# Kernel tuning notes

Hardware: AMD Instinct MI355X
Metric: run time of the kernel (lower is better)

Reference implementation:

```python
import jax, jax.numpy as jnp
import numpy as np

TEMPERATURE = 0.05
EPS = 1e-6
N, D = 8192, 64


def setup_inputs() -> dict:
    key = jax.random.key(0)
    k1, k2 = jax.random.split(key)
    anchor_embeddings = jax.random.normal(k1, (N, D), dtype=jnp.float32)
    positive_embeddings = jax.random.normal(k2, (N, D), dtype=jnp.float32)
    return {"anchor_embeddings": anchor_embeddings,
            "positive_embeddings": positive_embeddings}


def _cos_matrix(x, y, nx, ny):
    # pairwise cosine sim with torch CosineSimilarity eps semantics:
    # dot / max(||x||*||y||, eps)
    return (x @ y.T) / jnp.maximum(nx[:, None] * ny[None, :], EPS)


def reference(anchor_embeddings, positive_embeddings):
    a, p = anchor_embeddings, positive_embeddings
    na = jnp.linalg.norm(a, axis=-1)  # [N]
    npn = jnp.linalg.norm(p, axis=-1)  # [N]

    inv_t = 1.0 / TEMPERATURE
    S_ap = _cos_matrix(a, p, na, npn)  # [N, N]
    S_aa = _cos_matrix(a, a, na, na)   # [N, N]
    S_pp = _cos_matrix(p, p, npn, npn)  # [N, N]

    E_ap = jnp.exp(S_ap * inv_t)
    E_aa = jnp.exp(S_aa * inv_t)
    E_pp = jnp.exp(S_pp * inv_t)

    self_term = jnp.exp(jnp.asarray(inv_t, dtype=a.dtype))  # exp(1/T)
    # partition_i = sum_j E_ap[i,j] + sum_j E_aa[i,j] - e^{1/T}
    #             + sum_j E_ap[j,i] + sum_j E_pp[j,i] - e^{1/T}
    partition = (E_ap.sum(axis=1) + E_aa.sum(axis=1)
                 + E_ap.sum(axis=0) + E_pp.sum(axis=0)
                 - 2.0 * self_term)

    # loss = -mean_i log( exp(cos(a_i,p_i)/T) / partition_i )
    pos_logit = jnp.diagonal(S_ap) * inv_t
    loss = -jnp.mean(pos_logit - jnp.log(partition))
    return loss
```

## Files before the change

kernel.cpp:

```cpp
#include <hip/hip_runtime.h>
#include <hip/hip_bf16.h>
#include <math.h>

#define N 8192
#define D 64
#define INVT 20.0f
#define EPS 1e-6f
#define ZSCALE 5.3715835f

typedef __attribute__((ext_vector_type(8))) short bf16x8;
typedef __attribute__((ext_vector_type(4))) float f32x4;

#if __has_builtin(__builtin_amdgcn_exp2f)
#define EXP2F(x) __builtin_amdgcn_exp2f(x)
#else
#define EXP2F(x) exp2f(x)
#endif


__device__ __forceinline__ void unrank(int t, int& bi, int& bj) {
    int b = (int)((257.0f - sqrtf(66049.0f - 8.0f * (float)t)) * 0.5f);
    while (b * (257 - b) / 2 > t) --b;
    while ((b + 1) * (256 - b) / 2 <= t) ++b;
    bi = b;
    bj = b + (t - b * (257 - b) / 2);
}

__global__ __launch_bounds__(256) void prep_kernel(
    const float* __restrict__ A, const float* __restrict__ P,
    __hip_bfloat16* __restrict__ Zn, float* __restrict__ diag20,
    float* __restrict__ part, float* __restrict__ lacc, unsigned* __restrict__ cnt) {
    if (blockIdx.x < 64) part[blockIdx.x * 256 + threadIdx.x] = 0.0f;
    else if (blockIdx.x == 64 && threadIdx.x == 0) { *lacc = 0.0f; *cnt = 0u; }

    const int lane = threadIdx.x & 63;
    const int w    = threadIdx.x >> 6;
    const int r    = blockIdx.x * 4 + w;
    const int u    = lane >> 3, sub = lane & 7;
    const int upos = (u >> 2) * 64 + (u & 3) * 16;

    float a = A[r * D + lane];
    float p = P[r * D + lane];
    float sa = a * a, sp = p * p, dp = a * p;
    #pragma unroll
    for (int off = 1; off < 64; off <<= 1) {
        sa += __shfl_xor(sa, off, 64);
        sp += __shfl_xor(sp, off, 64);
        dp += __shfl_xor(dp, off, 64);
    }
    float na  = sqrtf(sa);
    float npn = sqrtf(sp);
    {
        int g = r >> 4, l2 = r & 15;
        Zn[(g * 128 + upos + l2) * 8 + sub] = __float2bfloat16(a * (ZSCALE / na));
    }
    {
        int R = N + r; int g = R >> 4, l2 = R & 15;
        Zn[(g * 128 + upos + l2) * 8 + sub] = __float2bfloat16(p * (ZSCALE / npn));
    }
    if (lane == 0)
        diag20[r] = (dp / fmaxf(na * npn, EPS)) * INVT;
}

__global__ __launch_bounds__(256, 4) void tiles_kernel(
    const __hip_bfloat16* __restrict__ Zn, float* __restrict__ part) {
    __shared__ float rs[4][16][68];
    __shared__ float merged[2][128];
    __shared__ float cmerged[2][2][64];

    const int tid = threadIdx.x;
    const int lane = tid & 63, w = tid >> 6;
    const int wr = w >> 1, wc = w & 1;
    const int ln = lane & 15, q = lane >> 4;
    const bf16x8* Zf = (const bf16x8*)Zn;

    int bi0, bj0, bi1, bj1;
    unrank(2 * (int)blockIdx.x,     bi0, bj0);
    unrank(2 * (int)blockIdx.x + 1, bi1, bj1);

    const f32x4 zero = {0.0f, 0.0f, 0.0f, 0.0f};

    bf16x8 af0[4][2], bv0[4][2];
    #pragma unroll
    for (int ii = 0; ii < 4; ++ii) {
        int ga = bi0 * 8 + wr * 4 + ii;
        int gb = bj0 * 8 + wc * 4 + ii;
        #pragma unroll
        for (int kc = 0; kc < 2; ++kc) {
            af0[ii][kc] = Zf[ga * 128 + kc * 64 + lane];
            bv0[ii][kc] = Zf[gb * 128 + kc * 64 + lane];
        }
    }

    const bool dwave0 = (bi0 == bj0) && (wr == wc);
    float csum[4] = {0.0f, 0.0f, 0.0f, 0.0f};
    #pragma unroll
    for (int ii = 0; ii < 4; ++ii) {
        f32x4 acc[4];
        #pragma unroll
        for (int jj = 0; jj < 4; ++jj)
            acc[jj] = __builtin_amdgcn_mfma_f32_16x16x32_bf16(
                af0[ii][0], bv0[jj][0], zero, 0, 0, 0);
        #pragma unroll
        for (int jj = 0; jj < 4; ++jj)
            acc[jj] = __builtin_amdgcn_mfma_f32_16x16x32_bf16(
                af0[ii][1], bv0[jj][1], acc[jj], 0, 0, 0);

        f32x4 rsum_ii = {};
        #pragma unroll
        for (int jj = 0; jj < 4; ++jj) {
            f32x4 e;
            #pragma unroll
            for (int r = 0; r < 4; ++r) e[r] = EXP2F(acc[jj][r]);
            if (dwave0 && (ii == jj)) {
                #pragma unroll
                for (int r = 0; r < 4; ++r)
                    if (ln == q * 4 + r) e[r] = 0.0f;
            }
            rsum_ii += e;
            csum[jj] += (e[0] + e[1]) + (e[2] + e[3]);
        }
        *(f32x4*)&rs[w][ln][ii * 16 + q * 4] = rsum_ii;
    }

    bf16x8 af1[4][2], bv1[4][2];
    #pragma unroll
    for (int ii = 0; ii < 4; ++ii) {
        int ga = bi1 * 8 + wr * 4 + ii;
        int gb = bj1 * 8 + wc * 4 + ii;
        #pragma unroll
        for (int kc = 0; kc < 2; ++kc) {
            af1[ii][kc] = Zf[ga * 128 + kc * 64 + lane];
            bv1[ii][kc] = Zf[gb * 128 + kc * 64 + lane];
        }
    }

    {
        float rowsum = 0.0f;
        #pragma unroll
        for (int l = 0; l < 16; ++l) rowsum += rs[w][l][lane];
        merged[wc][wr * 64 + lane] = rowsum;

        float cs0 = csum[0], cs1 = csum[1], cs2 = csum[2], cs3 = csum[3];
        cs0 += __shfl_xor(cs0, 16, 64); cs0 += __shfl_xor(cs0, 32, 64);
        cs1 += __shfl_xor(cs1, 16, 64); cs1 += __shfl_xor(cs1, 32, 64);
        cs2 += __shfl_xor(cs2, 16, 64); cs2 += __shfl_xor(cs2, 32, 64);
        cs3 += __shfl_xor(cs3, 16, 64); cs3 += __shfl_xor(cs3, 32, 64);
        float cval = (q == 0) ? cs0 : (q == 1) ? cs1 : (q == 2) ? cs2 : cs3;
        cmerged[wr][wc][q * 16 + ln] = cval;
        __syncthreads();

        if (tid < 128) {
            atomicAdd(part + bi0 * 128 + tid, merged[0][tid] + merged[1][tid]);
        } else if (bi0 != bj0) {
            int col = tid - 128;
            atomicAdd(part + bj0 * 128 + col,
                      cmerged[0][col >> 6][col & 63] + cmerged[1][col >> 6][col & 63]);
        }
    }
    __syncthreads();

    const bool dwave1 = (bi1 == bj1) && (wr == wc);
    float csumB[4] = {0.0f, 0.0f, 0.0f, 0.0f};
    #pragma unroll
    for (int ii = 0; ii < 4; ++ii) {
        f32x4 acc[4];
        #pragma unroll
        for (int jj = 0; jj < 4; ++jj)
            acc[jj] = __builtin_amdgcn_mfma_f32_16x16x32_bf16(
                af1[ii][0], bv1[jj][0], zero, 0, 0, 0);
        #pragma unroll
        for (int jj = 0; jj < 4; ++jj)
            acc[jj] = __builtin_amdgcn_mfma_f32_16x16x32_bf16(
                af1[ii][1], bv1[jj][1], acc[jj], 0, 0, 0);

        f32x4 rsum_ii = {};
        #pragma unroll
        for (int jj = 0; jj < 4; ++jj) {
            f32x4 e;
            #pragma unroll
            for (int r = 0; r < 4; ++r) e[r] = EXP2F(acc[jj][r]);
            if (dwave1 && (ii == jj)) {
                #pragma unroll
                for (int r = 0; r < 4; ++r)
                    if (ln == q * 4 + r) e[r] = 0.0f;
            }
            rsum_ii += e;
            csumB[jj] += (e[0] + e[1]) + (e[2] + e[3]);
        }
        *(f32x4*)&rs[w][ln][ii * 16 + q * 4] = rsum_ii;
    }

    {
        float rowsum = 0.0f;
        #pragma unroll
        for (int l = 0; l < 16; ++l) rowsum += rs[w][l][lane];
        merged[wc][wr * 64 + lane] = rowsum;

        float cs0 = csumB[0], cs1 = csumB[1], cs2 = csumB[2], cs3 = csumB[3];
        cs0 += __shfl_xor(cs0, 16, 64); cs0 += __shfl_xor(cs0, 32, 64);
        cs1 += __shfl_xor(cs1, 16, 64); cs1 += __shfl_xor(cs1, 32, 64);
        cs2 += __shfl_xor(cs2, 16, 64); cs2 += __shfl_xor(cs2, 32, 64);
        cs3 += __shfl_xor(cs3, 16, 64); cs3 += __shfl_xor(cs3, 32, 64);
        float cval = (q == 0) ? cs0 : (q == 1) ? cs1 : (q == 2) ? cs2 : cs3;
        cmerged[wr][wc][q * 16 + ln] = cval;
        __syncthreads();

        if (tid < 128) {
            atomicAdd(part + bi1 * 128 + tid, merged[0][tid] + merged[1][tid]);
        } else if (bi1 != bj1) {
            int col = tid - 128;
            atomicAdd(part + bj1 * 128 + col,
                      cmerged[0][col >> 6][col & 63] + cmerged[1][col >> 6][col & 63]);
        }
    }
}

__global__ __launch_bounds__(256) void loss_kernel(
    const float* __restrict__ part, const float* __restrict__ diag20,
    float* __restrict__ lacc, unsigned* __restrict__ cnt, float* __restrict__ out) {
    int i = blockIdx.x * 256 + threadIdx.x;
    float v = logf(part[i] + part[N + i]) - diag20[i];
    #pragma unroll
    for (int off = 32; off > 0; off >>= 1) v += __shfl_down(v, off, 64);
    __shared__ float wsm[4];
    int lane = threadIdx.x & 63, wv = threadIdx.x >> 6;
    if (lane == 0) wsm[wv] = v;
    __syncthreads();
    if (threadIdx.x == 0) {
        atomicAdd(lacc, wsm[0] + wsm[1] + wsm[2] + wsm[3]);
        __threadfence();
        unsigned old = atomicAdd(cnt, 1u);
        if (old == (N / 256 - 1)) {
            float tot = atomicAdd(lacc, 0.0f);
            out[0] = tot * (1.0f / (float)N);
        }
    }
}

extern "C" void kernel_launch(void* const* d_in, const int* in_sizes, int n_in,
                              void* d_out, int out_size, void* d_ws, size_t ws_size,
                              hipStream_t stream) {
    const float* A = (const float*)d_in[0];
    const float* P = (const float*)d_in[1];

    __hip_bfloat16* Zn = (__hip_bfloat16*)d_ws;
    float* diag20 = (float*)((char*)d_ws + 2u * N * D * sizeof(__hip_bfloat16));
    float* part   = diag20 + N;
    float* lacc   = part + 2 * N;
    unsigned* cnt = (unsigned*)(lacc + 1);

    prep_kernel<<<N / 4, 256, 0, stream>>>(A, P, Zn, diag20, part, lacc, cnt);

    const int nblocks = 128 * 129 / 4;
    tiles_kernel<<<nblocks, 256, 0, stream>>>(Zn, part);

    loss_kernel<<<N / 256, 256, 0, stream>>>(part, diag20, lacc, cnt, (float*)d_out);
}
```

Measured before the change: 91.77 us.

## Persistent blocks walk consecutive upper-triangle tiles, reusing A fragments and row sums

Instead of each block handling two arbitrary triangle tiles, 1024 blocks each process 8 or 9 consecutive tiles in row-major triangle order. The A-row fragments and row-sum accumulators stay in registers across tiles of the same block-row, so row atomics are flushed only at row boundaries. Column sums are now atomically added directly per wave, without LDS merging. This cuts redundant A loads, LDS traffic and row atomics, but tiles within a block run serially, block work is uneven at row wraps, and there are more column atomics.

After: 112.7 us. 1.23x slower.

```diff
diff --git a/kernel.cpp b/kernel.cpp
--- a/kernel.cpp
+++ b/kernel.cpp
@@ -66,154 +66,119 @@
     const __hip_bfloat16* __restrict__ Zn, float* __restrict__ part) {
     __shared__ float rs[4][16][68];
     __shared__ float merged[2][128];
-    __shared__ float cmerged[2][2][64];
 
     const int tid = threadIdx.x;
     const int lane = tid & 63, w = tid >> 6;
     const int wr = w >> 1, wc = w & 1;
     const int ln = lane & 15, q = lane >> 4;
     const bf16x8* Zf = (const bf16x8*)Zn;
-
-    int bi0, bj0, bi1, bj1;
-    unrank(2 * (int)blockIdx.x,     bi0, bj0);
-    unrank(2 * (int)blockIdx.x + 1, bi1, bj1);
-
     const f32x4 zero = {0.0f, 0.0f, 0.0f, 0.0f};
 
-    bf16x8 af0[4][2], bv0[4][2];
+    const int b = (int)blockIdx.x;
+    const int ntiles = (b < 64) ? 9 : 8;
+    int bi, bj;
+    unrank(b * 8 + ((b < 64) ? b : 64), bi, bj);
+
+    bf16x8 af[4][2];
     #pragma unroll
     for (int ii = 0; ii < 4; ++ii) {
-        int ga = bi0 * 8 + wr * 4 + ii;
-        int gb = bj0 * 8 + wc * 4 + ii;
+        int ga = bi * 8 + wr * 4 + ii;
+        af[ii][0] = Zf[ga * 128 + lane];
+        af[ii][1] = Zf[ga * 128 + 64 + lane];
+    }
+
+    float rsum[4][4] = {{0.0f}};
+
+    for (int t = 0; t < ntiles; ++t) {
+        bf16x8 bv[4][2];
         #pragma unroll
-        for (int kc = 0; kc < 2; ++kc) {
-            af0[ii][kc] = Zf[ga * 128 + kc * 64 + lane];
-            bv0[ii][kc] = Zf[gb * 128 + kc * 64 + lane];
-        }
-    }
-
-    const bool dwave0 = (bi0 == bj0) && (wr == wc);
-    float csum[4] = {0.0f, 0.0f, 0.0f, 0.0f};
-    #pragma unroll
-    for (int ii = 0; ii < 4; ++ii) {
-        f32x4 acc[4];
+        for (int ii = 0; ii < 4; ++ii) {
+            int gb = bj * 8 + wc * 4 + ii;
+            bv[ii][0] = Zf[gb * 128 + lane];
+            bv[ii][1] = Zf[gb * 128 + 64 + lane];
+        }
+
+        const bool dwave = (bi == bj) && (wr == wc);
+        float csum[4] = {0.0f, 0.0f, 0.0f, 0.0f};
         #pragma unroll
-        for (int jj = 0; jj < 4; ++jj)
-            acc[jj] = __builtin_amdgcn_mfma_f32_16x16x32_bf16(
-                af0[ii][0], bv0[jj][0], zero, 0, 0, 0);
-        #pragma unroll
-        for (int jj = 0; jj < 4; ++jj)
-            acc[jj] = __builtin_amdgcn_mfma_f32_16x16x32_bf16(
-                af0[ii][1], bv0[jj][1], acc[jj], 0, 0, 0);
-
-        f32x4 rsum_ii = {};
-        #pragma unroll
-        for (int jj = 0; jj < 4; ++jj) {
-            f32x4 e;
+        for (int ii = 0; ii < 4; ++ii) {
+            f32x4 acc[4];
             #pragma unroll
-            for (int r = 0; r < 4; ++r) e[r] = EXP2F(acc[jj][r]);
-            if (dwave0 && (ii == jj)) {
-                #pragma unroll
-                for (int r = 0; r < 4; ++r)
-                    if (ln == q * 4 + r) e[r] = 0.0f;
+            for (int jj = 0; jj < 4; ++jj)
+                acc[jj] = __builtin_amdgcn_mfma_f32_16x16x32_bf16(
+                    af[ii][0], bv[jj][0], zero, 0, 0, 0);
+            #pragma unroll
+            for (int jj = 0; jj < 4; ++jj)
+                acc[jj] = __builtin_amdgcn_mfma_f32_16x16x32_bf16(
+                    af[ii][1], bv[jj][1], acc[jj], 0, 0, 0);
+
+            #pragma unroll
+            for (int jj = 0; jj < 4; ++jj) {
+                f32x4 e;
+                #pragma unroll
+                for (int r = 0; r < 4; ++r) e[r] = EXP2F(acc[jj][r]);
+                if (dwave && (ii == jj)) {
+                    #pragma unroll
+                    for (int r = 0; r < 4; ++r)
+                        if (ln == q * 4 + r) e[r] = 0.0f;
+                }
+                #pragma unroll
+                for (int r = 0; r < 4; ++r) rsum[ii][r] += e[r];
+                csum[jj] += (e[0] + e[1]) + (e[2] + e[3]);
             }
-            rsum_ii += e;
-            csum[jj] += (e[0] + e[1]) + (e[2] + e[3]);
-        }
-        *(f32x4*)&rs[w][ln][ii * 16 + q * 4] = rsum_ii;
-    }
-
-    bf16x8 af1[4][2], bv1[4][2];
-    #pragma unroll
-    for (int ii = 0; ii < 4; ++ii) {
-        int ga = bi1 * 8 + wr * 4 + ii;
-        int gb = bj1 * 8 + wc * 4 + ii;
-        #pragma unroll
-        for (int kc = 0; kc < 2; ++kc) {
-            af1[ii][kc] = Zf[ga * 128 + kc * 64 + lane];
-            bv1[ii][kc] = Zf[gb * 128 + kc * 64 + lane];
-        }
-    }
-
-    {
-        float rowsum = 0.0f;
-        #pragma unroll
-        for (int l = 0; l < 16; ++l) rowsum += rs[w][l][lane];
-        merged[wc][wr * 64 + lane] = rowsum;
-
-        float cs0 = csum[0], cs1 = csum[1], cs2 = csum[2], cs3 = csum[3];
-        cs0 += __shfl_xor(cs0, 16, 64); cs0 += __shfl_xor(cs0, 32, 64);
-        cs1 += __shfl_xor(cs1, 16, 64); cs1 += __shfl_xor(cs1, 32, 64);
-        cs2 += __shfl_xor(cs2, 16, 64); cs2 += __shfl_xor(cs2, 32, 64);
-        cs3 += __shfl_xor(cs3, 16, 64); cs3 += __shfl_xor(cs3, 32, 64);
-        float cval = (q == 0) ? cs0 : (q == 1) ? cs1 : (q == 2) ? cs2 : cs3;
-        cmerged[wr][wc][q * 16 + ln] = cval;
-        __syncthreads();
-
-        if (tid < 128) {
-            atomicAdd(part + bi0 * 128 + tid, merged[0][tid] + merged[1][tid]);
-        } else if (bi0 != bj0) {
-            int col = tid - 128;
-            atomicAdd(part + bj0 * 128 + col,
-                      cmerged[0][col >> 6][col & 63] + cmerged[1][col >> 6][col & 63]);
-        }
-    }
+        }
+
+        if (bi != bj) {
+            float cs0 = csum[0], cs1 = csum[1], cs2 = csum[2], cs3 = csum[3];
+            cs0 += __shfl_xor(cs0, 16, 64); cs0 += __shfl_xor(cs0, 32, 64);
+            cs1 += __shfl_xor(cs1, 16, 64); cs1 += __shfl_xor(cs1, 32, 64);
+            cs2 += __shfl_xor(cs2, 16, 64); cs2 += __shfl_xor(cs2, 32, 64);
+            cs3 += __shfl_xor(cs3, 16, 64); cs3 += __shfl_xor(cs3, 32, 64);
+            float cval = (q == 0) ? cs0 : (q == 1) ? cs1 : (q == 2) ? cs2 : cs3;
+            atomicAdd(part + bj * 128 + wc * 64 + lane, cval);
+        }
+
+        if (t + 1 < ntiles) {
+            if (bj == 127) {
+                #pragma unroll
+                for (int ii = 0; ii < 4; ++ii)
+                    *(f32x4*)&rs[w][ln][ii * 16 + q * 4] = *(const f32x4*)&rsum[ii][0];
+                float rowsum = 0.0f;
+                #pragma unroll
+                for (int l = 0; l < 16; ++l) rowsum += rs[w][l][lane];
+                merged[wc][wr * 64 + lane] = rowsum;
+                __syncthreads();
+                if (tid < 128)
+                    atomicAdd(part + bi * 128 + tid, merged[0][tid] + merged[1][tid]);
+                __syncthreads();
+                #pragma unroll
+                for (int ii = 0; ii < 4; ++ii) {
+                    #pragma unroll
+                    for (int r = 0; r < 4; ++r) rsum[ii][r] = 0.0f;
+                }
+                ++bi; bj = bi;
+                #pragma unroll
+                for (int ii = 0; ii < 4; ++ii) {
+                    int ga = bi * 8 + wr * 4 + ii;
+                    af[ii][0] = Zf[ga * 128 + lane];
+                    af[ii][1] = Zf[ga * 128 + 64 + lane];
+                }
+            } else {
+                ++bj;
+            }
+        }
+    }
+
+    #pragma unroll
+    for (int ii = 0; ii < 4; ++ii)
+        *(f32x4*)&rs[w][ln][ii * 16 + q * 4] = *(const f32x4*)&rsum[ii][0];
+    float rowsum = 0.0f;
+    #pragma unroll
+    for (int l = 0; l < 16; ++l) rowsum += rs[w][l][lane];
+    merged[wc][wr * 64 + lane] = rowsum;
     __syncthreads();
-
-    const bool dwave1 = (bi1 == bj1) && (wr == wc);
-    float csumB[4] = {0.0f, 0.0f, 0.0f, 0.0f};
-    #pragma unroll
-    for (int ii = 0; ii < 4; ++ii) {
-        f32x4 acc[4];
-        #pragma unroll
-        for (int jj = 0; jj < 4; ++jj)
-            acc[jj] = __builtin_amdgcn_mfma_f32_16x16x32_bf16(
-                af1[ii][0], bv1[jj][0], zero, 0, 0, 0);
-        #pragma unroll
-        for (int jj = 0; jj < 4; ++jj)
-            acc[jj] = __builtin_amdgcn_mfma_f32_16x16x32_bf16(
-                af1[ii][1], bv1[jj][1], acc[jj], 0, 0, 0);
-
-        f32x4 rsum_ii = {};
-        #pragma unroll
-        for (int jj = 0; jj < 4; ++jj) {
-            f32x4 e;
-            #pragma unroll
-            for (int r = 0; r < 4; ++r) e[r] = EXP2F(acc[jj][r]);
-            if (dwave1 && (ii == jj)) {
-                #pragma unroll
-                for (int r = 0; r < 4; ++r)
-                    if (ln == q * 4 + r) e[r] = 0.0f;
-            }
-            rsum_ii += e;
-            csumB[jj] += (e[0] + e[1]) + (e[2] + e[3]);
-        }
-        *(f32x4*)&rs[w][ln][ii * 16 + q * 4] = rsum_ii;
-    }
-
-    {
-        float rowsum = 0.0f;
-        #pragma unroll
-        for (int l = 0; l < 16; ++l) rowsum += rs[w][l][lane];
-        merged[wc][wr * 64 + lane] = rowsum;
-
-        float cs0 = csumB[0], cs1 = csumB[1], cs2 = csumB[2], cs3 = csumB[3];
-        cs0 += __shfl_xor(cs0, 16, 64); cs0 += __shfl_xor(cs0, 32, 64);
-        cs1 += __shfl_xor(cs1, 16, 64); cs1 += __shfl_xor(cs1, 32, 64);
-        cs2 += __shfl_xor(cs2, 16, 64); cs2 += __shfl_xor(cs2, 32, 64);
-        cs3 += __shfl_xor(cs3, 16, 64); cs3 += __shfl_xor(cs3, 32, 64);
-        float cval = (q == 0) ? cs0 : (q == 1) ? cs1 : (q == 2) ? cs2 : cs3;
-        cmerged[wr][wc][q * 16 + ln] = cval;
-        __syncthreads();
-
-        if (tid < 128) {
-            atomicAdd(part + bi1 * 128 + tid, merged[0][tid] + merged[1][tid]);
-        } else if (bi1 != bj1) {
-            int col = tid - 128;
-            atomicAdd(part + bj1 * 128 + col,
-                      cmerged[0][col >> 6][col & 63] + cmerged[1][col >> 6][col & 63]);
-        }
-    }
+    if (tid < 128)
+        atomicAdd(part + bi * 128 + tid, merged[0][tid] + merged[1][tid]);
 }
 
 __global__ __launch_bounds__(256) void loss_kernel(
@@ -252,8 +217,7 @@
 
     prep_kernel<<<N / 4, 256, 0, stream>>>(A, P, Zn, diag20, part, lacc, cnt);
 
-    const int nblocks = 128 * 129 / 4;
-    tiles_kernel<<<nblocks, 256, 0, stream>>>(Zn, part);
+    tiles_kernel<<<1024, 256, 0, stream>>>(Zn, part);
 
     loss_kernel<<<N / 256, 256, 0, stream>>>(part, diag20, lacc, cnt, (float*)d_out);
 }
```

## Replace tile atomics with per-tile partial buffers and a deterministic reduce kernel

Applied to the files above, without the earlier changes.

Each tile block now writes its row and column partial sums to dedicated per-tile slots instead of doing atomicAdd into a shared partition array. A new reduce kernel sums those slots for each of the 16384 partition entries, and the zero-initialisation of the partition in prep is dropped. This is meant to remove contention from many blocks atomically updating the same addresses. In exchange it adds a fourth kernel launch and about 8 MB of extra global traffic, and the reduce loops are serial per thread with up to 128 iterations.

Result: slower. 107.5 us (+17.1%).

```diff
diff --git a/kernel.cpp b/kernel.cpp
--- a/kernel.cpp
+++ b/kernel.cpp
@@ -7,6 +7,7 @@
 #define INVT 20.0f
 #define EPS 1e-6f
 #define ZSCALE 5.3715835f
+#define NTILES 8256
 
 typedef __attribute__((ext_vector_type(8))) short bf16x8;
 typedef __attribute__((ext_vector_type(4))) float f32x4;
@@ -29,9 +30,8 @@
 __global__ __launch_bounds__(256) void prep_kernel(
     const float* __restrict__ A, const float* __restrict__ P,
     __hip_bfloat16* __restrict__ Zn, float* __restrict__ diag20,
-    float* __restrict__ part, float* __restrict__ lacc, unsigned* __restrict__ cnt) {
-    if (blockIdx.x < 64) part[blockIdx.x * 256 + threadIdx.x] = 0.0f;
-    else if (blockIdx.x == 64 && threadIdx.x == 0) { *lacc = 0.0f; *cnt = 0u; }
+    float* __restrict__ lacc, unsigned* __restrict__ cnt) {
+    if (blockIdx.x == 0 && threadIdx.x == 0) { *lacc = 0.0f; *cnt = 0u; }
 
     const int lane = threadIdx.x & 63;
     const int w    = threadIdx.x >> 6;
@@ -63,7 +63,8 @@
 }
 
 __global__ __launch_bounds__(256, 4) void tiles_kernel(
-    const __hip_bfloat16* __restrict__ Zn, float* __restrict__ part) {
+    const __hip_bfloat16* __restrict__ Zn,
+    float* __restrict__ rowbuf, float* __restrict__ colbuf) {
     __shared__ float rs[4][16][68];
     __shared__ float merged[2][128];
     __shared__ float cmerged[2][2][64];
@@ -74,9 +75,11 @@
     const int ln = lane & 15, q = lane >> 4;
     const bf16x8* Zf = (const bf16x8*)Zn;
 
+    const int t0 = 2 * (int)blockIdx.x;
+    const int t1 = t0 + 1;
     int bi0, bj0, bi1, bj1;
-    unrank(2 * (int)blockIdx.x,     bi0, bj0);
-    unrank(2 * (int)blockIdx.x + 1, bi1, bj1);
+    unrank(t0, bi0, bj0);
+    unrank(t1, bi1, bj1);
 
     const f32x4 zero = {0.0f, 0.0f, 0.0f, 0.0f};
 
@@ -151,11 +154,11 @@
         __syncthreads();
 
         if (tid < 128) {
-            atomicAdd(part + bi0 * 128 + tid, merged[0][tid] + merged[1][tid]);
+            rowbuf[t0 * 128 + tid] = merged[0][tid] + merged[1][tid];
         } else if (bi0 != bj0) {
             int col = tid - 128;
-            atomicAdd(part + bj0 * 128 + col,
-                      cmerged[0][col >> 6][col & 63] + cmerged[1][col >> 6][col & 63]);
+            colbuf[t0 * 128 + col] =
+                cmerged[0][col >> 6][col & 63] + cmerged[1][col >> 6][col & 63];
         }
     }
     __syncthreads();
@@ -207,13 +210,31 @@
         __syncthreads();
 
         if (tid < 128) {
-            atomicAdd(part + bi1 * 128 + tid, merged[0][tid] + merged[1][tid]);
+            rowbuf[t1 * 128 + tid] = merged[0][tid] + merged[1][tid];
         } else if (bi1 != bj1) {
             int col = tid - 128;
-            atomicAdd(part + bj1 * 128 + col,
-                      cmerged[0][col >> 6][col & 63] + cmerged[1][col >> 6][col & 63]);
-        }
-    }
+            colbuf[t1 * 128 + col] =
+                cmerged[0][col >> 6][col & 63] + cmerged[1][col >> 6][col & 63];
+        }
+    }
+}
+
+__global__ __launch_bounds__(256) void reduce_kernel(
+    const float* __restrict__ rowbuf, const float* __restrict__ colbuf,
+    float* __restrict__ part) {
+    const int R  = (int)blockIdx.x * 256 + (int)threadIdx.x;
+    const int bi = R >> 7, c = R & 127;
+    const int base = bi * (257 - bi) / 2;
+
+    float s = 0.0f;
+    const int nrow = 128 - bi;
+    #pragma unroll 4
+    for (int k = 0; k < nrow; ++k)
+        s += rowbuf[(base + k) * 128 + c];
+    #pragma unroll 4
+    for (int r = 0; r < bi; ++r)
+        s += colbuf[(r * (257 - r) / 2 + (bi - r)) * 128 + c];
+    part[R] = s;
 }
 
 __global__ __launch_bounds__(256) void loss_kernel(
@@ -246,14 +267,17 @@
 
     __hip_bfloat16* Zn = (__hip_bfloat16*)d_ws;
     float* diag20 = (float*)((char*)d_ws + 2u * N * D * sizeof(__hip_bfloat16));
-    float* part   = diag20 + N;
+    float* rowbuf = diag20 + N;
+    float* colbuf = rowbuf + NTILES * 128;
+    float* part   = colbuf + NTILES * 128;
     float* lacc   = part + 2 * N;
     unsigned* cnt = (unsigned*)(lacc + 1);
 
-    prep_kernel<<<N / 4, 256, 0, stream>>>(A, P, Zn, diag20, part, lacc, cnt);
-
-    const int nblocks = 128 * 129 / 4;
-    tiles_kernel<<<nblocks, 256, 0, stream>>>(Zn, part);
+    prep_kernel<<<N / 4, 256, 0, stream>>>(A, P, Zn, diag20, lacc, cnt);
+
+    tiles_kernel<<<NTILES / 2, 256, 0, stream>>>(Zn, rowbuf, colbuf);
+
+    reduce_kernel<<<2 * N / 256, 256, 0, stream>>>(rowbuf, colbuf, part);
 
     loss_kernel<<<N / 256, 256, 0, stream>>>(part, diag20, lacc, cnt, (float*)d_out);
 }
```
